# Performance work log

Hardware: AMD Instinct MI355X
Metric: run time of the kernel (lower is better)

Reference implementation:

```python
import jax, jax.numpy as jnp
import numpy as np

B = 2
N = 300000
C_IN = 2
PC = (-75.2, -75.2, 75.2, 75.2)
BEV = 0.8
GRID = int(round((PC[2] - PC[0]) / BEV))  # 188
CH = 256


def setup_inputs() -> dict:
    key = jax.random.key(0)
    ks = jax.random.split(key, 8)
    xy = jax.random.uniform(ks[0], (N, 2), minval=PC[0], maxval=PC[2], dtype=jnp.float32)
    z = jax.random.uniform(ks[1], (N, 1), minval=-2.0, maxval=4.0, dtype=jnp.float32)
    xyz = jnp.concatenate([xy, z], axis=-1)
    xyz_batch_cnt = jnp.full((B,), N // B, dtype=jnp.int32)
    pt_features = jax.random.normal(ks[2], (N, C_IN), dtype=jnp.float32)
    mlp_w = jax.random.normal(ks[3], (6 + C_IN, CH), dtype=jnp.float32) * 0.1
    mlp_g = jnp.ones((CH,), jnp.float32)
    mlp_b = jnp.zeros((CH,), jnp.float32)
    conv4_w = jax.random.normal(ks[4], (5, 3, 3, CH, CH), dtype=jnp.float32) * 0.02
    conv4_g = jnp.ones((5, CH), jnp.float32)
    conv4_b = jnp.zeros((5, CH), jnp.float32)
    conv5_w = jax.random.normal(ks[5], (5, 3, 3, CH, CH), dtype=jnp.float32) * 0.02
    conv5_g = jnp.ones((5, CH), jnp.float32)
    conv5_b = jnp.zeros((5, CH), jnp.float32)
    return dict(xyz=xyz, pt_features=pt_features, xyz_batch_cnt=xyz_batch_cnt,
                mlp_w=mlp_w, mlp_g=mlp_g, mlp_b=mlp_b,
                conv4_w=conv4_w, conv4_g=conv4_g, conv4_b=conv4_b,
                conv5_w=conv5_w, conv5_g=conv5_g, conv5_b=conv5_b)


def _conv(x, w, stride=1):
    # NHWC input, HWIO kernel, torch padding=1
    return jax.lax.conv_general_dilated(x, w, (stride, stride), [(1, 1), (1, 1)],
                                        dimension_numbers=("NHWC", "HWIO", "NHWC"))


def _bn(x, g, b):
    # eval-mode BatchNorm folded into per-channel affine
    return x * g + b


def _forward(xyz, pt_features, xyz_batch_cnt, mlp_w, mlp_g, mlp_b,
             conv4_w, conv4_g, conv4_b, conv5_w, conv5_g, conv5_b):
    n = xyz.shape[0]
    batch_idx = jnp.repeat(jnp.arange(B, dtype=jnp.int32), xyz_batch_cnt, total_repeat_length=n)
    ix = jnp.clip(jnp.floor((xyz[:, 0] - PC[0]) / BEV).astype(jnp.int32), 0, GRID - 1)
    iy = jnp.clip(jnp.floor((xyz[:, 1] - PC[1]) / BEV).astype(jnp.int32), 0, GRID - 1)
    cx = PC[0] + (ix.astype(xyz.dtype) + 0.5) * BEV
    cy = PC[1] + (iy.astype(xyz.dtype) + 0.5) * BEV
    # 6 geometric features (xyz + offsets to pillar center) + raw point features
    feat = jnp.concatenate([xyz,
                            (xyz[:, 0] - cx)[:, None],
                            (xyz[:, 1] - cy)[:, None],
                            xyz[:, 2:3],
                            pt_features], axis=-1)  # [N, 8]
    h = jax.nn.relu(_bn(feat @ mlp_w, mlp_g, mlp_b))  # [N, 256]
    flat = (batch_idx * GRID + iy) * GRID + ix  # [N]
    grid = jnp.full((B * GRID * GRID, CH), -jnp.inf, h.dtype).at[flat].max(h)
    occ = jnp.zeros((B * GRID * GRID, 1), h.dtype).at[flat].set(1.0)
    x = jnp.where(occ > 0, grid, 0.0).reshape(B, GRID, GRID, CH)
    mask = occ.reshape(B, GRID, GRID, 1)
    relu = jax.nn.relu
    # Sparse2DBasicBlockV (submanifold convs == dense conv on zero-padded grid + active-site mask)
    x0 = mask * relu(_bn(_conv(x, conv4_w[0]), conv4_g[0], conv4_b[0]))
    out = mask * relu(_bn(_conv(x0, conv4_w[1]), conv4_g[1], conv4_b[1]))
    out = mask * _bn(_conv(out, conv4_w[2]), conv4_g[2], conv4_b[2])
    x1 = relu(out + x0)
    # Sparse2DBasicBlock
    out = mask * relu(_bn(_conv(x1, conv4_w[3]), conv4_g[3], conv4_b[3]))
    out = mask * _bn(_conv(out, conv4_w[4]), conv4_g[4], conv4_b[4])
    x_conv4 = relu(out + x1)  # [B, 188, 188, 256]
    # conv5: strided dense conv + 2 Dense2DBasicBlocks
    y = relu(_bn(_conv(x_conv4, conv5_w[0], stride=2), conv5_g[0], conv5_b[0]))  # [B, 94, 94, 256]
    for i in (1, 3):
        out = relu(_bn(_conv(y, conv5_w[i]), conv5_g[i], conv5_b[i]))
        out = _bn(_conv(out, conv5_w[i + 1]), conv5_g[i + 1], conv5_b[i + 1])
        y = relu(out + y)
    return (jnp.transpose(x_conv4, (0, 3, 1, 2)), jnp.transpose(y, (0, 3, 1, 2)))


def reference(xyz, pt_features, xyz_batch_cnt, mlp_w, mlp_g, mlp_b,
              conv4_w, conv4_g, conv4_b, conv5_w, conv5_g, conv5_b):
    return _forward(xyz, pt_features, xyz_batch_cnt, mlp_w, mlp_g, mlp_b,
                    conv4_w, conv4_g, conv4_b, conv5_w, conv5_g, conv5_b)
```

## Files before the change

kernel.cpp:

```cpp
#include <hip/hip_runtime.h>
#include <hip/hip_bf16.h>


typedef __attribute__((ext_vector_type(8))) short bf16x8;
typedef __attribute__((ext_vector_type(4))) float f32x4;
typedef unsigned short u16;

#define GLD16(g, l)                                                   \
    __builtin_amdgcn_global_load_lds(                                 \
        (const __attribute__((address_space(1))) void*)(g),           \
        (__attribute__((address_space(3))) void*)(l), 16, 0, 0)

#define SB0 __builtin_amdgcn_sched_barrier(0)
#define MFMA16(a, b, c) __builtin_amdgcn_mfma_f32_16x16x32_bf16((a), (b), (c), 0, 0, 0)

__device__ __forceinline__ u16 f2b(float f) {
    unsigned u = __float_as_uint(f);
    u += 0x7fffu + ((u >> 16) & 1u);
    return (u16)(u >> 16);
}
__device__ __forceinline__ float b2f(u16 h) {
    return __uint_as_float(((unsigned)h) << 16);
}

__global__ __launch_bounds__(256) void bin_kernel(
    const float* __restrict__ xyz, const int* __restrict__ cnt,
    int* __restrict__ pcnt, int* __restrict__ plist, int N) {
    int i = blockIdx.x * 256 + threadIdx.x;
    if (i >= N) return;
    float x = xyz[3 * i], y = xyz[3 * i + 1];
    int b = (i < cnt[0]) ? 0 : 1;
    int ix = (int)floorf((x + 75.2f) / 0.8f);
    int iy = (int)floorf((y + 75.2f) / 0.8f);
    ix = min(max(ix, 0), 187);
    iy = min(max(iy, 0), 187);
    int flat = (b * 188 + iy) * 188 + ix;
    int slot = atomicAdd(pcnt + flat, 1);
    if (slot < 32) plist[flat * 32 + slot] = i;
}

__global__ __launch_bounds__(256) void pillar_kernel(
    const float* __restrict__ xyz, const float* __restrict__ ptf,
    const float* __restrict__ mw, const float* __restrict__ mg,
    const float* __restrict__ mb, const int* __restrict__ pcnt,
    const int* __restrict__ plist, u16* __restrict__ out,
    float* __restrict__ occ) {
    const int lane = threadIdx.x & 63, wid = threadIdx.x >> 6;
    const int p = blockIdx.x * 4 + wid;
    const int n = min(pcnt[p], 32);
    const int c = lane * 4;
    float m0 = 0.f, m1 = 0.f, m2 = 0.f, m3 = 0.f;
    if (n > 0) {
        const int ix = p % 188;
        const int iy = (p / 188) % 188;
        const float cx = -75.2f + ((float)ix + 0.5f) * 0.8f;
        const float cy = -75.2f + ((float)iy + 0.5f) * 0.8f;
        float4 w[8];
#pragma unroll
        for (int k = 0; k < 8; k++) w[k] = *(const float4*)(mw + k * 256 + c);
        for (int t = 0; t < n; t++) {
            int i = __builtin_amdgcn_readfirstlane(plist[p * 32 + t]);
            float x = xyz[3 * i], y = xyz[3 * i + 1], z = xyz[3 * i + 2];
            float f0 = ptf[2 * i], f1 = ptf[2 * i + 1];
            const float f[8] = {x, y, z, x - cx, y - cy, z, f0, f1};
            float s0 = 0.f, s1 = 0.f, s2 = 0.f, s3 = 0.f;
#pragma unroll
            for (int k = 0; k < 8; k++) {
                s0 = fmaf(f[k], w[k].x, s0);
                s1 = fmaf(f[k], w[k].y, s1);
                s2 = fmaf(f[k], w[k].z, s2);
                s3 = fmaf(f[k], w[k].w, s3);
            }
            float4 g4 = *(const float4*)(mg + c);
            float4 b4 = *(const float4*)(mb + c);
            m0 = fmaxf(m0, fmaxf(s0 * g4.x + b4.x, 0.f));
            m1 = fmaxf(m1, fmaxf(s1 * g4.y + b4.y, 0.f));
            m2 = fmaxf(m2, fmaxf(s2 * g4.z + b4.z, 0.f));
            m3 = fmaxf(m3, fmaxf(s3 * g4.w + b4.w, 0.f));
        }
    }
    unsigned lo = (unsigned)f2b(m0) | ((unsigned)f2b(m1) << 16);
    unsigned hi = (unsigned)f2b(m2) | ((unsigned)f2b(m3) << 16);
    *(uint2*)(out + (size_t)p * 256 + c) = make_uint2(lo, hi);
    if (lane == 0) occ[p] = (n > 0) ? 1.f : 0.f;
}

__global__ __launch_bounds__(256) void cvt_weights_kernel(
    const float* __restrict__ w4, const float* __restrict__ w5,
    u16* __restrict__ wt4, u16* __restrict__ wt5) {
    int g = blockIdx.x * 256 + threadIdx.x;
    int mat = g >> 13;
    int r = g & 8191;
    int nb = r >> 11;
    int kc = (r >> 9) & 3;
    int kh = (r >> 8) & 1;
    int nf = (r >> 6) & 3;
    int lane = r & 63;
    int c0 = kc * 64 + kh * 32 + (lane >> 4) * 8;
    int n = nb * 64 + nf * 16 + (lane & 15);
    const float* src = (mat < 45) ? (w4 + (size_t)mat * 65536)
                                  : (w5 + (size_t)(mat - 45) * 65536);
    u16* dst = ((mat < 45) ? (wt4 + (size_t)mat * 65536)
                           : (wt5 + (size_t)(mat - 45) * 65536)) +
               (size_t)r * 8;
    u16 v[8];
#pragma unroll
    for (int e = 0; e < 8; e++) v[e] = f2b(src[(c0 + e) * 256 + n]);
    *(uint4*)dst = *(const uint4*)v;
}

template <int STRIDE, bool HAS_MASK, bool HAS_RES, bool HAS_F32OUT>
__global__ __launch_bounds__(256, 2) void conv3x3_kernel(
    const u16* __restrict__ in, const u16* __restrict__ wt,
    const u16* __restrict__ zeros, const float* __restrict__ gamma,
    const float* __restrict__ beta, const float* __restrict__ mask,
    const u16* __restrict__ res, u16* __restrict__ outb,
    float* __restrict__ outf, int Hin, int Win, int Hout, int Wout, int Bn) {
    const int M = Bn * Hout * Wout;
    const int HWo = Hout * Wout;
    const int HWi = Hin * Win;
    const int tid = threadIdx.x;
    const int lane = tid & 63, wid = tid >> 6;
    const int wr = wid >> 1, wc = wid & 1;
    const int nwg = gridDim.x;
    const int q = nwg >> 3, r = nwg & 7;
    const int xc = blockIdx.x & 7, jj = blockIdx.x >> 3;
    const int wg = (xc < r ? xc * (q + 1) : r * (q + 1) + (xc - r) * q) + jj;
    const int m0 = (wg >> 1) * 128;
    const int n0 = (wg & 1) * 128;

    __shared__ u16 SMEM[24576];
    const int lrow = lane >> 3;
    const int csw = (((lane & 7) ^ (lrow & 7)) << 3);

    int ppy[4], ppx[4], ppb[4];
    bool ppo[4];
#pragma unroll
    for (int j = 0; j < 4; j++) {
        int gp = m0 + wid * 32 + j * 8 + lrow;
        ppo[j] = gp < M;
        int g2 = ppo[j] ? gp : 0;
        int b = g2 / HWo;
        int rr = g2 - b * HWo;
        ppy[j] = rr / Wout;
        ppx[j] = rr - ppy[j] * Wout;
        ppb[j] = b;
    }
    const int nb = (n0 >> 6) + wc;
    const u16* wb = wt + (size_t)nb * 16384 + lane * 8;

#define MKPTR(dst, T)                                                         \
    do {                                                                      \
        int dy_ = (T) / 3 - 1, dx_ = (T) % 3 - 1;                             \
        _Pragma("unroll") for (int j = 0; j < 4; j++) {                       \
            int sy_ = ppy[j] * STRIDE + dy_;                                  \
            int sx_ = ppx[j] * STRIDE + dx_;                                  \
            bool ok_ = ppo[j] && sy_ >= 0 && sy_ < Hin && sx_ >= 0 &&         \
                       sx_ < Win;                                             \
            long long off_ =                                                  \
                ((long long)ppb[j] * HWi + (long long)sy_ * Win + sx_) * 256; \
            dst[j] = ok_ ? in + off_ + csw : zeros + csw;                     \
        }                                                                     \
    } while (0)

#define ISSUE_A(APTR, KC, SLOT)                                               \
    do {                                                                      \
        u16* dA_ = SMEM + (SLOT)*8192;                                        \
        _Pragma("unroll") for (int j = 0; j < 4; j++) {                       \
            GLD16(APTR[j] + (KC)*64, dA_ + (wid * 32 + j * 8) * 64);          \
        }                                                                     \
    } while (0)

#define LOADB(SET, tt, kk)                                                    \
    do {                                                                      \
        const u16* base_ = wb + (tt)*65536 + (kk)*4096;                       \
        SET##0 = *(const bf16x8*)(base_);                                     \
        SET##1 = *(const bf16x8*)(base_ + 2048);                              \
        SET##2 = *(const bf16x8*)(base_ + 512);                               \
        SET##3 = *(const bf16x8*)(base_ + 2560);                              \
        SET##4 = *(const bf16x8*)(base_ + 1024);                              \
        SET##5 = *(const bf16x8*)(base_ + 3072);                              \
        SET##6 = *(const bf16x8*)(base_ + 1536);                              \
        SET##7 = *(const bf16x8*)(base_ + 3584);                              \
    } while (0)

#define STEPC(SET)                                                            \
    do {                                                                      \
        bf16x8 af_[4];                                                        \
        _Pragma("unroll") for (int m_ = 0; m_ < 4; m_++) af_[m_] =            \
            *(const bf16x8*)(Ar + (wr * 64 + m_ * 16 + rA) * 64 + (kb ^ xk)); \
        __builtin_amdgcn_s_setprio(1);                                        \
        _Pragma("unroll") for (int m_ = 0; m_ < 4; m_++) {                    \
            acc[m_][0] = MFMA16(af_[m_], SET##0, acc[m_][0]);                 \
            acc[m_][1] = MFMA16(af_[m_], SET##2, acc[m_][1]);                 \
            acc[m_][2] = MFMA16(af_[m_], SET##4, acc[m_][2]);                 \
            acc[m_][3] = MFMA16(af_[m_], SET##6, acc[m_][3]);                 \
        }                                                                     \
        __builtin_amdgcn_s_setprio(0);                                        \
        _Pragma("unroll") for (int m_ = 0; m_ < 4; m_++) af_[m_] =            \
            *(const bf16x8*)(Ar + (wr * 64 + m_ * 16 + rA) * 64 +             \
                             ((32 + kb) ^ xk));                               \
        __builtin_amdgcn_s_setprio(1);                                        \
        _Pragma("unroll") for (int m_ = 0; m_ < 4; m_++) {                    \
            acc[m_][0] = MFMA16(af_[m_], SET##1, acc[m_][0]);                 \
            acc[m_][1] = MFMA16(af_[m_], SET##3, acc[m_][1]);                 \
            acc[m_][2] = MFMA16(af_[m_], SET##5, acc[m_][2]);                 \
            acc[m_][3] = MFMA16(af_[m_], SET##7, acc[m_][3]);                 \
        }                                                                     \
        __builtin_amdgcn_s_setprio(0);                                        \
    } while (0)

    f32x4 acc[4][4];
#pragma unroll
    for (int m = 0; m < 4; m++)
#pragma unroll
        for (int n = 0; n < 4; n++) acc[m][n] = (f32x4)0.f;

    const int rA = lane & 15;
    const int kb = (lane >> 4) * 8;
    const int xk = (rA & 7) << 3;

    bf16x8 bA0, bA1, bA2, bA3, bA4, bA5, bA6, bA7;
    bf16x8 bB0, bB1, bB2, bB3, bB4, bB5, bB6, bB7;

    const u16* aptrc[4];
    const u16* aptrn[4];
    MKPTR(aptrc, 0);
    ISSUE_A(aptrc, 0, 0);
    SB0;
    LOADB(bA, 0, 0);
    SB0;
    ISSUE_A(aptrc, 1, 1);
    SB0;
    LOADB(bB, 0, 1);
    SB0;

    int b0 = 0;

#pragma unroll 1
    for (int t = 0; t < 9; t++) {
        MKPTR(aptrn, t + 1);
#pragma unroll
        for (int kc = 0; kc < 4; kc++) {
            const int s = t * 4 + kc;
            int ib = b0 + kc;
            if (ib >= 3) ib -= 3;
            if (s < 35) {
                asm volatile("s_waitcnt vmcnt(12)" ::: "memory");
            } else {
                asm volatile("s_waitcnt vmcnt(0)" ::: "memory");
            }
            SB0;
            __builtin_amdgcn_s_barrier();
            SB0;
            if (s < 34) {
                int ia = ib + 2;
                if (ia >= 3) ia -= 3;
                if (kc < 2) {
                    ISSUE_A(aptrc, kc + 2, ia);
                } else {
                    ISSUE_A(aptrn, kc - 2, ia);
                }
            }
            SB0;
            const u16* Ar = SMEM + ib * 8192;
            if (kc & 1) {
                STEPC(bB);
            } else {
                STEPC(bA);
            }
            SB0;
            if (s < 34) {
                const int tB = (kc < 2) ? t : t + 1;
                const int kB = (kc < 2) ? kc + 2 : kc - 2;
                if (kc & 1) {
                    LOADB(bB, tB, kB);
                } else {
                    LOADB(bA, tB, kB);
                }
            }
            SB0;
        }
#pragma unroll
        for (int j = 0; j < 4; j++) aptrc[j] = aptrn[j];
        b0 = (b0 == 2) ? 0 : b0 + 1;
    }

    __syncthreads();
    float* ep = (float*)SMEM + wid * 2112;
    const int cb = n0 + wc * 64;
    float gms[4], bts[4];
#pragma unroll
    for (int n = 0; n < 4; n++) {
        gms[n] = gamma[cb + n * 16 + rA];
        bts[n] = beta[cb + n * 16 + rA];
    }
#pragma unroll
    for (int half = 0; half < 2; half++) {
#pragma unroll
        for (int m2 = 0; m2 < 2; m2++) {
            const int m = half * 2 + m2;
            const int lrb = m2 * 16 + ((lane >> 4) << 2);
            const int gpb = m0 + wr * 64 + half * 32 + lrb;
#pragma unroll
            for (int rr = 0; rr < 4; rr++) {
                float mk = 1.f;
                if (HAS_MASK) mk = (gpb + rr < M) ? mask[gpb + rr] : 0.f;
#pragma unroll
                for (int n = 0; n < 4; n++) {
                    float v = acc[m][n][rr] * gms[n] + bts[n];
                    if (HAS_MASK) v *= mk;
                    ep[(lrb + rr) * 66 + n * 16 + rA] = v;
                }
            }
        }
#pragma unroll
        for (int i = 0; i < 8; i++) {
            const int lr = i * 4 + (lane >> 4);
            const int gp = m0 + wr * 64 + half * 32 + lr;
            f32x4 v = *(const f32x4*)(ep + lr * 66 + rA * 4);
            if (HAS_RES && gp < M) {
                uint2 rv = *(const uint2*)(res + (size_t)gp * 256 + cb + rA * 4);
                v[0] += b2f((u16)(rv.x & 0xffff));
                v[1] += b2f((u16)(rv.x >> 16));
                v[2] += b2f((u16)(rv.y & 0xffff));
                v[3] += b2f((u16)(rv.y >> 16));
            }
            v[0] = fmaxf(v[0], 0.f);
            v[1] = fmaxf(v[1], 0.f);
            v[2] = fmaxf(v[2], 0.f);
            v[3] = fmaxf(v[3], 0.f);
            if (HAS_F32OUT) *(f32x4*)(ep + lr * 66 + rA * 4) = v;
            if (gp < M) {
                unsigned lo = (unsigned)f2b(v[0]) | ((unsigned)f2b(v[1]) << 16);
                unsigned hi = (unsigned)f2b(v[2]) | ((unsigned)f2b(v[3]) << 16);
                *(uint2*)(outb + (size_t)gp * 256 + cb + rA * 4) =
                    make_uint2(lo, hi);
            }
        }
        if (HAS_F32OUT) {
#pragma unroll
            for (int i = 0; i < 16; i++) {
                const int lc = i * 4 + (lane >> 4);
                const int p0 = rA * 2;
                const int gp0 = m0 + wr * 64 + half * 32 + p0;
                if (gp0 < M) {
                    float v0 = ep[p0 * 66 + lc];
                    float v1 = ep[(p0 + 1) * 66 + lc];
                    int b = gp0 / HWo;
                    int rr = gp0 - b * HWo;
                    const int ch = cb + lc;
                    float* o = outf + ((size_t)(b * 256 + ch)) * HWo + rr;
                    *(float2*)o = make_float2(v0, v1);
                }
            }
        }
    }
#undef MKPTR
#undef ISSUE_A
#undef LOADB
#undef STEPC
}

extern "C" void kernel_launch(void* const* d_in, const int* in_sizes, int n_in,
                              void* d_out, int out_size, void* d_ws,
                              size_t ws_size, hipStream_t stream) {
    const float* xyz = (const float*)d_in[0];
    const float* ptf = (const float*)d_in[1];
    const int* cnt = (const int*)d_in[2];
    const float* mw = (const float*)d_in[3];
    const float* mg = (const float*)d_in[4];
    const float* mb = (const float*)d_in[5];
    const float* c4w = (const float*)d_in[6];
    const float* c4g = (const float*)d_in[7];
    const float* c4b = (const float*)d_in[8];
    const float* c5w = (const float*)d_in[9];
    const float* c5g = (const float*)d_in[10];
    const float* c5b = (const float*)d_in[11];
    const int N = in_sizes[0] / 3;

    char* ws = (char*)d_ws;
    int* pcnt = (int*)ws;
    u16* zeros = (u16*)(ws + 282752);
    float* occ = (float*)(ws + 283264);
    int* plist = (int*)(ws + 566016);
    u16* wt4 = (u16*)(ws + 9614080);
    u16* wt5 = (u16*)(ws + 15512320);
    u16* bufA = (u16*)(ws + 21410560);
    u16* bufB = (u16*)(ws + 57602816);
    u16* bufC = (u16*)(ws + 93795072);

    float* outXC4 = (float*)d_out;
    float* outY = ((float*)d_out) + 18096128;

    const int M188 = 2 * 188 * 188;
    const int M94 = 2 * 94 * 94;

    hipMemsetAsync(ws, 0, 283264, stream);
    cvt_weights_kernel<<<2880, 256, 0, stream>>>(c4w, c5w, wt4, wt5);
    bin_kernel<<<(N + 255) / 256, 256, 0, stream>>>(xyz, cnt, pcnt, plist, N);
    pillar_kernel<<<M188 / 4, 256, 0, stream>>>(xyz, ptf, mw, mg, mb, pcnt,
                                                plist, bufA, occ);

    dim3 g188(2 * ((M188 + 127) / 128)), g94(2 * ((M94 + 127) / 128));
    const size_t WL = 9 * 65536;

    conv3x3_kernel<1, true, false, false><<<g188, 256, 0, stream>>>(
        bufA, wt4 + 0 * WL, zeros, c4g + 0, c4b + 0, occ, nullptr, bufB,
        nullptr, 188, 188, 188, 188, 2);
    conv3x3_kernel<1, true, false, false><<<g188, 256, 0, stream>>>(
        bufB, wt4 + 1 * WL, zeros, c4g + 256, c4b + 256, occ, nullptr, bufC,
        nullptr, 188, 188, 188, 188, 2);
    conv3x3_kernel<1, true, true, false><<<g188, 256, 0, stream>>>(
        bufC, wt4 + 2 * WL, zeros, c4g + 512, c4b + 512, occ, bufB, bufA,
        nullptr, 188, 188, 188, 188, 2);
    conv3x3_kernel<1, true, false, false><<<g188, 256, 0, stream>>>(
        bufA, wt4 + 3 * WL, zeros, c4g + 768, c4b + 768, occ, nullptr, bufC,
        nullptr, 188, 188, 188, 188, 2);
    conv3x3_kernel<1, true, true, true><<<g188, 256, 0, stream>>>(
        bufC, wt4 + 4 * WL, zeros, c4g + 1024, c4b + 1024, occ, bufA, bufB,
        outXC4, 188, 188, 188, 188, 2);

    conv3x3_kernel<2, false, false, false><<<g94, 256, 0, stream>>>(
        bufB, wt5 + 0 * WL, zeros, c5g + 0, c5b + 0, nullptr, nullptr, bufA,
        nullptr, 188, 188, 94, 94, 2);
    conv3x3_kernel<1, false, false, false><<<g94, 256, 0, stream>>>(
        bufA, wt5 + 1 * WL, zeros, c5g + 256, c5b + 256, nullptr, nullptr,
        bufC, nullptr, 94, 94, 94, 94, 2);
    conv3x3_kernel<1, false, true, false><<<g94, 256, 0, stream>>>(
        bufC, wt5 + 2 * WL, zeros, c5g + 512, c5b + 512, nullptr, bufA, bufB,
        nullptr, 94, 94, 94, 94, 2);
    conv3x3_kernel<1, false, false, false><<<g94, 256, 0, stream>>>(
        bufB, wt5 + 3 * WL, zeros, c5g + 768, c5b + 768, nullptr, nullptr,
        bufC, nullptr, 94, 94, 94, 94, 2);
    conv3x3_kernel<1, false, true, true><<<g94, 256, 0, stream>>>(
        bufC, wt5 + 4 * WL, zeros, c5g + 1024, c5b + 1024, nullptr, bufB,
        bufA, outY, 94, 94, 94, 94, 2);
}
```

Baseline: 902.5 us.

## Widen conv tile to full 256 output channels with 512-thread workgroups

Each conv workgroup now covers all 256 output channels for 128 output pixels, using 8 waves (2 rows x 4 column groups) instead of 4 waves over a 128x128 tile. Each im2col A tile is loaded into LDS once and shared across all output channels instead of being fetched by two workgroups, which halves activation gather traffic. The epilogue is restructured per 16-row slice and the fp32 NCHW output switches to scalar stores. Doubling the block size may lower occupancy or raise register pressure under launch_bounds(512,2), and halves the grid size.

```diff
diff --git a/kernel.cpp b/kernel.cpp
--- a/kernel.cpp
+++ b/kernel.cpp
@@ -110,7 +110,7 @@
 }
 
 template <int STRIDE, bool HAS_MASK, bool HAS_RES, bool HAS_F32OUT>
-__global__ __launch_bounds__(256, 2) void conv3x3_kernel(
+__global__ __launch_bounds__(512, 2) void conv3x3_kernel(
     const u16* __restrict__ in, const u16* __restrict__ wt,
     const u16* __restrict__ zeros, const float* __restrict__ gamma,
     const float* __restrict__ beta, const float* __restrict__ mask,
@@ -121,23 +121,23 @@
     const int HWi = Hin * Win;
     const int tid = threadIdx.x;
     const int lane = tid & 63, wid = tid >> 6;
-    const int wr = wid >> 1, wc = wid & 1;
+    const int wr = wid >> 2, wc = wid & 3;
     const int nwg = gridDim.x;
     const int q = nwg >> 3, r = nwg & 7;
     const int xc = blockIdx.x & 7, jj = blockIdx.x >> 3;
     const int wg = (xc < r ? xc * (q + 1) : r * (q + 1) + (xc - r) * q) + jj;
-    const int m0 = (wg >> 1) * 128;
-    const int n0 = (wg & 1) * 128;
+    const int m0 = wg * 128;
 
     __shared__ u16 SMEM[24576];
-    const int lrow = lane >> 3;
-    const int csw = (((lane & 7) ^ (lrow & 7)) << 3);
-
-    int ppy[4], ppx[4], ppb[4];
-    bool ppo[4];
-#pragma unroll
-    for (int j = 0; j < 4; j++) {
-        int gp = m0 + wid * 32 + j * 8 + lrow;
+
+    const int srow = tid >> 3;
+    const int csw = (((tid & 7) ^ (srow & 7)) << 3);
+
+    int ppy[2], ppx[2], ppb[2];
+    bool ppo[2];
+#pragma unroll
+    for (int j = 0; j < 2; j++) {
+        int gp = m0 + srow + j * 64;
         ppo[j] = gp < M;
         int g2 = ppo[j] ? gp : 0;
         int b = g2 / HWo;
@@ -146,13 +146,12 @@
         ppx[j] = rr - ppy[j] * Wout;
         ppb[j] = b;
     }
-    const int nb = (n0 >> 6) + wc;
-    const u16* wb = wt + (size_t)nb * 16384 + lane * 8;
+    const u16* wb = wt + (size_t)wc * 16384 + lane * 8;
 
 #define MKPTR(dst, T)                                                         \
     do {                                                                      \
         int dy_ = (T) / 3 - 1, dx_ = (T) % 3 - 1;                             \
-        _Pragma("unroll") for (int j = 0; j < 4; j++) {                       \
+        _Pragma("unroll") for (int j = 0; j < 2; j++) {                       \
             int sy_ = ppy[j] * STRIDE + dy_;                                  \
             int sx_ = ppx[j] * STRIDE + dx_;                                  \
             bool ok_ = ppo[j] && sy_ >= 0 && sy_ < Hin && sx_ >= 0 &&         \
@@ -165,9 +164,9 @@
 
 #define ISSUE_A(APTR, KC, SLOT)                                               \
     do {                                                                      \
-        u16* dA_ = SMEM + (SLOT)*8192;                                        \
-        _Pragma("unroll") for (int j = 0; j < 4; j++) {                       \
-            GLD16(APTR[j] + (KC)*64, dA_ + (wid * 32 + j * 8) * 64);          \
+        _Pragma("unroll") for (int j = 0; j < 2; j++) {                       \
+            GLD16(APTR[j] + (KC)*64,                                          \
+                  SMEM + (SLOT)*8192 + j * 4096 + wid * 512);                 \
         }                                                                     \
     } while (0)
 
@@ -223,8 +222,8 @@
     bf16x8 bA0, bA1, bA2, bA3, bA4, bA5, bA6, bA7;
     bf16x8 bB0, bB1, bB2, bB3, bB4, bB5, bB6, bB7;
 
-    const u16* aptrc[4];
-    const u16* aptrn[4];
+    const u16* aptrc[2];
+    const u16* aptrn[2];
     MKPTR(aptrc, 0);
     ISSUE_A(aptrc, 0, 0);
     SB0;
@@ -246,7 +245,7 @@
             int ib = b0 + kc;
             if (ib >= 3) ib -= 3;
             if (s < 35) {
-                asm volatile("s_waitcnt vmcnt(12)" ::: "memory");
+                asm volatile("s_waitcnt vmcnt(10)" ::: "memory");
             } else {
                 asm volatile("s_waitcnt vmcnt(0)" ::: "memory");
             }
@@ -282,13 +281,15 @@
             SB0;
         }
 #pragma unroll
-        for (int j = 0; j < 4; j++) aptrc[j] = aptrn[j];
+        for (int j = 0; j < 2; j++) aptrc[j] = aptrn[j];
         b0 = (b0 == 2) ? 0 : b0 + 1;
     }
 
     __syncthreads();
-    float* ep = (float*)SMEM + wid * 2112;
-    const int cb = n0 + wc * 64;
+    float* ep = (float*)SMEM + wid * 1056;
+    const int cb = wc * 64;
+    const int R0 = m0 + wr * 64;
+    const int kq = lane >> 4;
     float gms[4], bts[4];
 #pragma unroll
     for (int n = 0; n < 4; n++) {
@@ -296,28 +297,24 @@
         bts[n] = beta[cb + n * 16 + rA];
     }
 #pragma unroll
-    for (int half = 0; half < 2; half++) {
-#pragma unroll
-        for (int m2 = 0; m2 < 2; m2++) {
-            const int m = half * 2 + m2;
-            const int lrb = m2 * 16 + ((lane >> 4) << 2);
-            const int gpb = m0 + wr * 64 + half * 32 + lrb;
-#pragma unroll
-            for (int rr = 0; rr < 4; rr++) {
-                float mk = 1.f;
-                if (HAS_MASK) mk = (gpb + rr < M) ? mask[gpb + rr] : 0.f;
-#pragma unroll
-                for (int n = 0; n < 4; n++) {
-                    float v = acc[m][n][rr] * gms[n] + bts[n];
-                    if (HAS_MASK) v *= mk;
-                    ep[(lrb + rr) * 66 + n * 16 + rA] = v;
-                }
+    for (int qm = 0; qm < 4; qm++) {
+        const int lrb = kq << 2;
+        const int gpb = R0 + qm * 16 + lrb;
+#pragma unroll
+        for (int rr = 0; rr < 4; rr++) {
+            float mk = 1.f;
+            if (HAS_MASK) mk = (gpb + rr < M) ? mask[gpb + rr] : 0.f;
+#pragma unroll
+            for (int n = 0; n < 4; n++) {
+                float v = acc[qm][n][rr] * gms[n] + bts[n];
+                if (HAS_MASK) v *= mk;
+                ep[(lrb + rr) * 66 + n * 16 + rA] = v;
             }
         }
 #pragma unroll
-        for (int i = 0; i < 8; i++) {
-            const int lr = i * 4 + (lane >> 4);
-            const int gp = m0 + wr * 64 + half * 32 + lr;
+        for (int i = 0; i < 4; i++) {
+            const int lr = i * 4 + kq;
+            const int gp = R0 + qm * 16 + lr;
             f32x4 v = *(const f32x4*)(ep + lr * 66 + rA * 4);
             if (HAS_RES && gp < M) {
                 uint2 rv = *(const uint2*)(res + (size_t)gp * 256 + cb + rA * 4);
@@ -339,19 +336,16 @@
             }
         }
         if (HAS_F32OUT) {
-#pragma unroll
-            for (int i = 0; i < 16; i++) {
-                const int lc = i * 4 + (lane >> 4);
-                const int p0 = rA * 2;
-                const int gp0 = m0 + wr * 64 + half * 32 + p0;
-                if (gp0 < M) {
-                    float v0 = ep[p0 * 66 + lc];
-                    float v1 = ep[(p0 + 1) * 66 + lc];
-                    int b = gp0 / HWo;
-                    int rr = gp0 - b * HWo;
+            const int gp0 = R0 + qm * 16 + rA;
+            if (gp0 < M) {
+                int b = gp0 / HWo;
+                int rrp = gp0 - b * HWo;
+#pragma unroll
+                for (int i = 0; i < 16; i++) {
+                    const int lc = i * 4 + kq;
                     const int ch = cb + lc;
-                    float* o = outf + ((size_t)(b * 256 + ch)) * HWo + rr;
-                    *(float2*)o = make_float2(v0, v1);
+                    outf[((size_t)(b * 256 + ch)) * HWo + rrp] =
+                        ep[rA * 66 + lc];
                 }
             }
         }
@@ -402,38 +396,39 @@
     pillar_kernel<<<M188 / 4, 256, 0, stream>>>(xyz, ptf, mw, mg, mb, pcnt,
                                                 plist, bufA, occ);
 
-    dim3 g188(2 * ((M188 + 127) / 128)), g94(2 * ((M94 + 127) / 128));
+    dim3 g188((M188 + 127) / 128);
+    dim3 g94((M94 + 127) / 128);
     const size_t WL = 9 * 65536;
 
-    conv3x3_kernel<1, true, false, false><<<g188, 256, 0, stream>>>(
+    conv3x3_kernel<1, true, false, false><<<g188, 512, 0, stream>>>(
         bufA, wt4 + 0 * WL, zeros, c4g + 0, c4b + 0, occ, nullptr, bufB,
         nullptr, 188, 188, 188, 188, 2);
-    conv3x3_kernel<1, true, false, false><<<g188, 256, 0, stream>>>(
+    conv3x3_kernel<1, true, false, false><<<g188, 512, 0, stream>>>(
         bufB, wt4 + 1 * WL, zeros, c4g + 256, c4b + 256, occ, nullptr, bufC,
         nullptr, 188, 188, 188, 188, 2);
-    conv3x3_kernel<1, true, true, false><<<g188, 256, 0, stream>>>(
+    conv3x3_kernel<1, true, true, false><<<g188, 512, 0, stream>>>(
         bufC, wt4 + 2 * WL, zeros, c4g + 512, c4b + 512, occ, bufB, bufA,
         nullptr, 188, 188, 188, 188, 2);
-    conv3x3_kernel<1, true, false, false><<<g188, 256, 0, stream>>>(
+    conv3x3_kernel<1, true, false, false><<<g188, 512, 0, stream>>>(
         bufA, wt4 + 3 * WL, zeros, c4g + 768, c4b + 768, occ, nullptr, bufC,
         nullptr, 188, 188, 188, 188, 2);
-    conv3x3_kernel<1, true, true, true><<<g188, 256, 0, stream>>>(
+    conv3x3_kernel<1, true, true, true><<<g188, 512, 0, stream>>>(
         bufC, wt4 + 4 * WL, zeros, c4g + 1024, c4b + 1024, occ, bufA, bufB,
         outXC4, 188, 188, 188, 188, 2);
 
-    conv3x3_kernel<2, false, false, false><<<g94, 256, 0, stream>>>(
+    conv3x3_kernel<2, false, false, false><<<g94, 512, 0, stream>>>(
         bufB, wt5 + 0 * WL, zeros, c5g + 0, c5b + 0, nullptr, nullptr, bufA,
         nullptr, 188, 188, 94, 94, 2);
-    conv3x3_kernel<1, false, false, false><<<g94, 256, 0, stream>>>(
+    conv3x3_kernel<1, false, false, false><<<g94, 512, 0, stream>>>(
         bufA, wt5 + 1 * WL, zeros, c5g + 256, c5b + 256, nullptr, nullptr,
         bufC, nullptr, 94, 94, 94, 94, 2);
-    conv3x3_kernel<1, false, true, false><<<g94, 256, 0, stream>>>(
+    conv3x3_kernel<1, false, true, false><<<g94, 512, 0, stream>>>(
         bufC, wt5 + 2 * WL, zeros, c5g + 512, c5b + 512, nullptr, bufA, bufB,
         nullptr, 94, 94, 94, 94, 2);
-    conv3x3_kernel<1, false, false, false><<<g94, 256, 0, stream>>>(
+    conv3x3_kernel<1, false, false, false><<<g94, 512, 0, stream>>>(
         bufB, wt5 + 3 * WL, zeros, c5g + 768, c5b + 768, nullptr, nullptr,
         bufC, nullptr, 94, 94, 94, 94, 2);
-    conv3x3_kernel<1, false, true, true><<<g94, 256, 0, stream>>>(
+    conv3x3_kernel<1, false, true, true><<<g94, 512, 0, stream>>>(
         bufC, wt5 + 4 * WL, zeros, c5g + 1024, c5b + 1024, nullptr, bufB,
         bufA, outY, 94, 94, 94, 94, 2);
 }
```

Result: slower. 973.3 us (+7.9%).
